# Performance work log

Measured on AMD Instinct MI355X. Metric: run time of the kernel, lower is better.

## Reference

```python
import jax, jax.numpy as jnp
import numpy as np

BLK = 128          # stk blocking
HID = 1024         # hidden_size
FFN = 4096         # ffn_hidden_size per expert
NE = 8             # moe_num_experts
TOK = 8192         # padded tokens (multiple of BLK)


def setup_inputs() -> dict:
    key = jax.random.key(0)
    k1, k2, k3 = jax.random.split(key, 3)
    x = jax.random.normal(k1, (TOK, HID), dtype=jnp.float32)
    w1 = jax.random.normal(k2, (NE * FFN, HID), dtype=jnp.float32) * 0.02
    n_row_blocks = TOK // BLK          # 64
    cols_per_expert = FFN // BLK       # 32
    # dMoE topology: each token row-block is assigned one expert; its nonzero
    # column blocks are all ffn blocks of that expert.
    expert_assign = jax.random.randint(k3, (n_row_blocks,), 0, NE)
    row_indices = jnp.repeat(jnp.arange(n_row_blocks), cols_per_expert)
    column_indices = (expert_assign[:, None] * cols_per_expert
                      + jnp.arange(cols_per_expert)[None, :]).reshape(-1)
    return {
        "x": x,
        "w1": w1,
        "row_indices": row_indices.astype(jnp.int32),     # [nnz]
        "column_indices": column_indices.astype(jnp.int32),  # [nnz]
        "block": BLK,
    }


def reference(x, w1, row_indices, column_indices, block):
    # sdd(x, w1.T, topo): out block k = x_block[row_indices[k]] @ w1_block[column_indices[k]].T
    hid = x.shape[1]
    xb = x.reshape(-1, block, hid)    # [n_row_blocks, blk, hid]
    wb = w1.reshape(-1, block, hid)   # [n_col_blocks, blk, hid]
    # [nnz, blk, blk] block-sparse data of the output matrix
    return jnp.einsum('kbh,kch->kbc', xb[row_indices], wb[column_indices])
```

## Files before the change

kernel.cpp:

```cpp
#include <hip/hip_runtime.h>
#include <hip/hip_bf16.h>
#include <stdint.h>

#define HID 1024
#define BLKDIM 128
#define BK 32
#define NK (HID / BK)

using short8 = __attribute__((ext_vector_type(8))) short;
using f32x4  = __attribute__((ext_vector_type(4))) float;

__device__ __forceinline__ uint32_t bfround(float f) {
    uint32_t u = __builtin_bit_cast(uint32_t, f);
    return (u + 0x7FFFu + ((u >> 16) & 1u)) >> 16;
}

__device__ __forceinline__ void gld16(const ushort* g, const ushort* lds_base) {
    __builtin_amdgcn_global_load_lds(
        (const __attribute__((address_space(1))) void*)g,
        (__attribute__((address_space(3))) void*)lds_base, 16, 0, 0);
}

__global__ __launch_bounds__(256)
void cvt_bf16_kernel(const float* __restrict__ src, uint4* __restrict__ dst, int n8) {
    int i = blockIdx.x * blockDim.x + threadIdx.x;
    if (i >= n8) return;
    const float4* s = reinterpret_cast<const float4*>(src) + (size_t)i * 2;
    float4 v0 = s[0], v1 = s[1];
    uint4 w;
    w.x = bfround(v0.x) | (bfround(v0.y) << 16);
    w.y = bfround(v0.z) | (bfround(v0.w) << 16);
    w.z = bfround(v1.x) | (bfround(v1.y) << 16);
    w.w = bfround(v1.z) | (bfround(v1.w) << 16);
    dst[i] = w;
}

__global__ __launch_bounds__(512, 2)
void sdd_pair_kernel(const ushort* __restrict__ xb, const ushort* __restrict__ wb,
                     const int* __restrict__ rind, const int* __restrict__ cind,
                     float* __restrict__ out) {
    __shared__ ushort sA[2][BLKDIM * BK];
    __shared__ ushort sB[2][2 * BLKDIM * BK];

    int g = blockIdx.x;
    const int nwg = gridDim.x;
    if ((nwg & 7) == 0) {
        const int cpx = nwg >> 3;
        g = (g & 7) * cpx + (g >> 3);
    }
    const int k0 = g * 2;
    const int r  = rind[k0];

    const int t = threadIdx.x;
    const int w = t >> 6;
    const int lane = t & 63;

    const int arow = w * 16 + (lane >> 2);
    const ushort* ag = xb + (size_t)(r * BLKDIM + arow) * HID + (lane & 3) * 8;
    const int brow0 = w * 32 + (lane >> 2);
    const int brow1 = brow0 + 16;
    const int cA = cind[k0 + (brow0 >> 7)];
    const int cB = cind[k0 + (brow1 >> 7)];
    const ushort* bg0 = wb + (size_t)(cA * BLKDIM + (brow0 & 127)) * HID + (lane & 3) * 8;
    const ushort* bg1 = wb + (size_t)(cB * BLKDIM + (brow1 & 127)) * HID + (lane & 3) * 8;

    const int wr = (w >> 2) * 64;
    const int wc = (w & 3) * 64;
    const int lr = lane & 15;
    const int lk = (lane >> 4) * 8;

    f32x4 acc[4][4];
#pragma unroll
    for (int m = 0; m < 4; ++m)
#pragma unroll
        for (int n = 0; n < 4; ++n)
            acc[m][n] = (f32x4){0.f, 0.f, 0.f, 0.f};

    auto stage = [&](int buf, int kt) {
        gld16(ag  + kt * BK, &sA[buf][w * 512]);
        gld16(bg0 + kt * BK, &sB[buf][w * 1024]);
        gld16(bg1 + kt * BK, &sB[buf][w * 1024 + 512]);
    };

    stage(0, 0);
    int cur = 0;
    for (int kt = 0; kt < NK; ++kt) {
        __syncthreads();
        if (kt + 1 < NK) stage(cur ^ 1, kt + 1);
        const ushort* sa = sA[cur];
        const ushort* sb = sB[cur];
        short8 aF[4], bF[4];
#pragma unroll
        for (int m = 0; m < 4; ++m)
            aF[m] = *reinterpret_cast<const short8*>(&sa[(wr + m * 16 + lr) * BK + lk]);
#pragma unroll
        for (int n = 0; n < 4; ++n)
            bF[n] = *reinterpret_cast<const short8*>(&sb[(wc + n * 16 + lr) * BK + lk]);
#pragma unroll
        for (int m = 0; m < 4; ++m)
#pragma unroll
            for (int n = 0; n < 4; ++n)
                acc[m][n] = __builtin_amdgcn_mfma_f32_16x16x32_bf16(aF[m], bF[n], acc[m][n], 0, 0, 0);
        cur ^= 1;
    }

    const int blk = (w & 3) >> 1;
    float* op = out + (size_t)(k0 + blk) * (BLKDIM * BLKDIM);
    const int colbase = (wc & 64) ? 64 : 0;
    const int rbase = wr + (lane >> 4) * 4;
#pragma unroll
    for (int m = 0; m < 4; ++m)
#pragma unroll
        for (int n = 0; n < 4; ++n) {
            const int col = colbase + n * 16 + lr;
#pragma unroll
            for (int j = 0; j < 4; ++j)
                op[(size_t)(rbase + m * 16 + j) * BLKDIM + col] = acc[m][n][j];
        }
}

__device__ __forceinline__ void store16f(ushort* dst, float4 v0, float4 v1, float4 v2, float4 v3) {
    uint4 w0, w1;
    w0.x = bfround(v0.x) | (bfround(v0.y) << 16);
    w0.y = bfround(v0.z) | (bfround(v0.w) << 16);
    w0.z = bfround(v1.x) | (bfround(v1.y) << 16);
    w0.w = bfround(v1.z) | (bfround(v1.w) << 16);
    w1.x = bfround(v2.x) | (bfround(v2.y) << 16);
    w1.y = bfround(v2.z) | (bfround(v2.w) << 16);
    w1.z = bfround(v3.x) | (bfround(v3.y) << 16);
    w1.w = bfround(v3.z) | (bfround(v3.w) << 16);
    uint4* d = reinterpret_cast<uint4*>(dst);
    d[0] = w0; d[1] = w1;
}

__global__ __launch_bounds__(256, 2)
void sdd_bf16_kernel(const float* __restrict__ x, const float* __restrict__ w1,
                     const int* __restrict__ rind, const int* __restrict__ cind,
                     float* __restrict__ out) {
    __shared__ ushort sA[2][BLKDIM * BK];
    __shared__ ushort sB[2][BLKDIM * BK];
    const int k = blockIdx.x;
    const int t = threadIdx.x;
    const int r = rind[k];
    const int c = cind[k];
    const float* Abase = x  + (size_t)r * BLKDIM * HID;
    const float* Bbase = w1 + (size_t)c * BLKDIM * HID;
    const int srow = t >> 1, shalf = t & 1;
    const float* aptr = Abase + (size_t)srow * HID + shalf * 16;
    const float* bptr = Bbase + (size_t)srow * HID + shalf * 16;
    const int soff = srow * BK + shalf * 16;
    const int wv = t >> 6, lane = t & 63;
    const int wr = (wv >> 1) * 64, wc = (wv & 1) * 64;
    const int lr = lane & 15, lk = (lane >> 4) * 8;
    f32x4 acc[4][4];
#pragma unroll
    for (int m = 0; m < 4; ++m)
#pragma unroll
        for (int n = 0; n < 4; ++n) acc[m][n] = (f32x4){0.f, 0.f, 0.f, 0.f};
    float4 ra[4], rb[4];
#pragma unroll
    for (int i = 0; i < 4; ++i) {
        ra[i] = *reinterpret_cast<const float4*>(aptr + i * 4);
        rb[i] = *reinterpret_cast<const float4*>(bptr + i * 4);
    }
    store16f(&sA[0][soff], ra[0], ra[1], ra[2], ra[3]);
    store16f(&sB[0][soff], rb[0], rb[1], rb[2], rb[3]);
    __syncthreads();
    for (int kt = 0; kt < NK; ++kt) {
        const int cur = kt & 1;
        if (kt + 1 < NK) {
            const float* ap = aptr + (kt + 1) * BK;
            const float* bp = bptr + (kt + 1) * BK;
#pragma unroll
            for (int i = 0; i < 4; ++i) {
                ra[i] = *reinterpret_cast<const float4*>(ap + i * 4);
                rb[i] = *reinterpret_cast<const float4*>(bp + i * 4);
            }
        }
        const ushort* sa = sA[cur];
        const ushort* sb = sB[cur];
        short8 aF[4], bF[4];
#pragma unroll
        for (int m = 0; m < 4; ++m) aF[m] = *reinterpret_cast<const short8*>(&sa[(wr + m * 16 + lr) * BK + lk]);
#pragma unroll
        for (int n = 0; n < 4; ++n) bF[n] = *reinterpret_cast<const short8*>(&sb[(wc + n * 16 + lr) * BK + lk]);
#pragma unroll
        for (int m = 0; m < 4; ++m)
#pragma unroll
            for (int n = 0; n < 4; ++n)
                acc[m][n] = __builtin_amdgcn_mfma_f32_16x16x32_bf16(aF[m], bF[n], acc[m][n], 0, 0, 0);
        if (kt + 1 < NK) {
            store16f(&sA[cur ^ 1][soff], ra[0], ra[1], ra[2], ra[3]);
            store16f(&sB[cur ^ 1][soff], rb[0], rb[1], rb[2], rb[3]);
        }
        __syncthreads();
    }
    float* op = out + (size_t)k * (BLKDIM * BLKDIM);
    const int rbase = wr + (lane >> 4) * 4;
#pragma unroll
    for (int m = 0; m < 4; ++m)
#pragma unroll
        for (int n = 0; n < 4; ++n) {
            const int col = wc + n * 16 + lr;
#pragma unroll
            for (int j = 0; j < 4; ++j)
                op[(size_t)(rbase + m * 16 + j) * BLKDIM + col] = acc[m][n][j];
        }
}

extern "C" void kernel_launch(void* const* d_in, const int* in_sizes, int n_in,
                              void* d_out, int out_size, void* d_ws, size_t ws_size,
                              hipStream_t stream) {
    const float* x  = (const float*)d_in[0];
    const float* w1 = (const float*)d_in[1];
    const int* ri   = (const int*)d_in[2];
    const int* ci   = (const int*)d_in[3];
    float* out      = (float*)d_out;
    const int nnz   = in_sizes[2];
    const int nx    = in_sizes[0];
    const int nw    = in_sizes[1];

    const size_t need = ((size_t)nx + (size_t)nw) * sizeof(ushort);
    if (ws_size >= need && (nnz & 1) == 0) {
        ushort* xb = (ushort*)d_ws;
        ushort* wb = xb + nx;
        const int nx8 = nx / 8, nw8 = nw / 8;
        hipLaunchKernelGGL(cvt_bf16_kernel, dim3((nx8 + 255) / 256), dim3(256), 0, stream,
                           x, (uint4*)xb, nx8);
        hipLaunchKernelGGL(cvt_bf16_kernel, dim3((nw8 + 255) / 256), dim3(256), 0, stream,
                           w1, (uint4*)wb, nw8);
        hipLaunchKernelGGL(sdd_pair_kernel, dim3(nnz / 2), dim3(512), 0, stream,
                           xb, wb, ri, ci, out);
    } else {
        hipLaunchKernelGGL(sdd_bf16_kernel, dim3(nnz), dim3(256), 0, stream,
                           x, w1, ri, ci, out);
    }
}
```

Baseline: 143.1 us.

## Triple-buffer LDS pipeline with BK=64, XOR swizzle and split MFMA phases

Reworks the pair GEMM kernel to a three-stage LDS ring with a K-tile of 64, prefetching two tiles ahead using direct global-to-LDS loads interleaved between two MFMA half-phases. An XOR swizzle on the loaded K chunk reduces LDS bank conflicts, and explicit vmcnt waits with raw s_barrier replace the per-iteration __syncthreads. s_setprio raises priority around the MFMA bursts. This roughly triples LDS use per workgroup (about 144KB), which may limit occupancy to one workgroup per CU despite launch bounds asking for two.

After: 155.0 us. +8.3%, slower.

```diff
diff --git a/kernel.cpp b/kernel.cpp
--- a/kernel.cpp
+++ b/kernel.cpp
@@ -4,8 +4,9 @@
 
 #define HID 1024
 #define BLKDIM 128
-#define BK 32
-#define NK (HID / BK)
+#define BKT 64
+#define NKT (HID / BKT)
+#define NBUF 3
 
 using short8 = __attribute__((ext_vector_type(8))) short;
 using f32x4  = __attribute__((ext_vector_type(4))) float;
@@ -36,11 +37,11 @@
 }
 
 __global__ __launch_bounds__(512, 2)
-void sdd_pair_kernel(const ushort* __restrict__ xb, const ushort* __restrict__ wb,
+void sdd_pipe_kernel(const ushort* __restrict__ xb, const ushort* __restrict__ wb,
                      const int* __restrict__ rind, const int* __restrict__ cind,
                      float* __restrict__ out) {
-    __shared__ ushort sA[2][BLKDIM * BK];
-    __shared__ ushort sB[2][2 * BLKDIM * BK];
+    __shared__ ushort sA[NBUF][BLKDIM * BKT];
+    __shared__ ushort sB[NBUF][2 * BLKDIM * BKT];
 
     int g = blockIdx.x;
     const int nwg = gridDim.x;
@@ -53,21 +54,25 @@
 
     const int t = threadIdx.x;
     const int w = t >> 6;
-    const int lane = t & 63;
-
-    const int arow = w * 16 + (lane >> 2);
-    const ushort* ag = xb + (size_t)(r * BLKDIM + arow) * HID + (lane & 3) * 8;
-    const int brow0 = w * 32 + (lane >> 2);
-    const int brow1 = brow0 + 16;
-    const int cA = cind[k0 + (brow0 >> 7)];
-    const int cB = cind[k0 + (brow1 >> 7)];
-    const ushort* bg0 = wb + (size_t)(cA * BLKDIM + (brow0 & 127)) * HID + (lane & 3) * 8;
-    const ushort* bg1 = wb + (size_t)(cB * BLKDIM + (brow1 & 127)) * HID + (lane & 3) * 8;
-
-    const int wr = (w >> 2) * 64;
-    const int wc = (w & 3) * 64;
-    const int lr = lane & 15;
-    const int lk = (lane >> 4) * 8;
+    const int l = t & 63;
+
+    const int kx = (((l & 7) ^ ((l >> 3) & 7)) * 8);
+    const ushort* agb = xb + (size_t)(r * BLKDIM + w * 16 + (l >> 3)) * HID + kx;
+    const int cblk = cind[k0 + (w >> 2)];
+    const ushort* bgb = wb + (size_t)(cblk * BLKDIM + ((w * 32) & 127) + (l >> 3)) * HID + kx;
+
+    const int wr   = (w >> 2) * 64;
+    const int wcol = (w & 3) * 64;
+    const int lr = l & 15;
+    const int s0 = (l >> 4) ^ (l & 7);
+    const int c0 = s0 * 8;
+    const int c1 = (s0 ^ 4) * 8;
+
+    int aoff[4], boff[4];
+#pragma unroll
+    for (int m = 0; m < 4; ++m) aoff[m] = (wr + m * 16 + lr) * BKT;
+#pragma unroll
+    for (int n = 0; n < 4; ++n) boff[n] = (wcol + n * 16 + lr) * BKT;
 
     f32x4 acc[4][4];
 #pragma unroll
@@ -76,38 +81,72 @@
         for (int n = 0; n < 4; ++n)
             acc[m][n] = (f32x4){0.f, 0.f, 0.f, 0.f};
 
-    auto stage = [&](int buf, int kt) {
-        gld16(ag  + kt * BK, &sA[buf][w * 512]);
-        gld16(bg0 + kt * BK, &sB[buf][w * 1024]);
-        gld16(bg1 + kt * BK, &sB[buf][w * 1024 + 512]);
+    auto stageA = [&](int b, int kt, int i) {
+        gld16(agb + (size_t)i * 8 * HID + kt * BKT, &sA[b][w * 1024 + i * 512]);
     };
-
-    stage(0, 0);
-    int cur = 0;
-    for (int kt = 0; kt < NK; ++kt) {
-        __syncthreads();
-        if (kt + 1 < NK) stage(cur ^ 1, kt + 1);
-        const ushort* sa = sA[cur];
-        const ushort* sb = sB[cur];
-        short8 aF[4], bF[4];
-#pragma unroll
-        for (int m = 0; m < 4; ++m)
-            aF[m] = *reinterpret_cast<const short8*>(&sa[(wr + m * 16 + lr) * BK + lk]);
-#pragma unroll
-        for (int n = 0; n < 4; ++n)
-            bF[n] = *reinterpret_cast<const short8*>(&sb[(wc + n * 16 + lr) * BK + lk]);
-#pragma unroll
-        for (int m = 0; m < 4; ++m)
+    auto stageB = [&](int b, int kt, int i) {
+        gld16(bgb + (size_t)i * 8 * HID + kt * BKT, &sB[b][w * 2048 + i * 512]);
+    };
+
+    stageA(0, 0, 0); stageA(0, 0, 1);
+    stageB(0, 0, 0); stageB(0, 0, 1); stageB(0, 0, 2); stageB(0, 0, 3);
+    stageA(1, 1, 0); stageA(1, 1, 1);
+    stageB(1, 1, 0); stageB(1, 1, 1); stageB(1, 1, 2); stageB(1, 1, 3);
+    asm volatile("s_waitcnt vmcnt(6)" ::: "memory");
+    __builtin_amdgcn_s_barrier();
+    __builtin_amdgcn_sched_barrier(0);
+
+    for (int kt = 0; kt < NKT; ++kt) {
+        const int cur = kt % 3;
+        const int nxt = (kt + 2) % 3;
+        const bool pre = (kt + 2) < NKT;
+        const ushort* sa = &sA[cur][0];
+        const ushort* sb = &sB[cur][0];
+
+        {
+            short8 aF[4], bF[4];
+#pragma unroll
+            for (int m = 0; m < 4; ++m)
+                aF[m] = *reinterpret_cast<const short8*>(&sa[aoff[m] + c0]);
 #pragma unroll
             for (int n = 0; n < 4; ++n)
-                acc[m][n] = __builtin_amdgcn_mfma_f32_16x16x32_bf16(aF[m], bF[n], acc[m][n], 0, 0, 0);
-        cur ^= 1;
+                bF[n] = *reinterpret_cast<const short8*>(&sb[boff[n] + c0]);
+            if (pre) { stageA(nxt, kt + 2, 0); stageB(nxt, kt + 2, 0); stageB(nxt, kt + 2, 1); }
+            __builtin_amdgcn_s_setprio(1);
+#pragma unroll
+            for (int m = 0; m < 4; ++m)
+#pragma unroll
+                for (int n = 0; n < 4; ++n)
+                    acc[m][n] = __builtin_amdgcn_mfma_f32_16x16x32_bf16(aF[m], bF[n], acc[m][n], 0, 0, 0);
+            __builtin_amdgcn_s_setprio(0);
+        }
+        {
+            short8 aF[4], bF[4];
+#pragma unroll
+            for (int m = 0; m < 4; ++m)
+                aF[m] = *reinterpret_cast<const short8*>(&sa[aoff[m] + c1]);
+#pragma unroll
+            for (int n = 0; n < 4; ++n)
+                bF[n] = *reinterpret_cast<const short8*>(&sb[boff[n] + c1]);
+            if (pre) { stageA(nxt, kt + 2, 1); stageB(nxt, kt + 2, 2); stageB(nxt, kt + 2, 3); }
+            __builtin_amdgcn_s_setprio(1);
+#pragma unroll
+            for (int m = 0; m < 4; ++m)
+#pragma unroll
+                for (int n = 0; n < 4; ++n)
+                    acc[m][n] = __builtin_amdgcn_mfma_f32_16x16x32_bf16(aF[m], bF[n], acc[m][n], 0, 0, 0);
+            __builtin_amdgcn_s_setprio(0);
+        }
+        if (pre) asm volatile("s_waitcnt vmcnt(6)" ::: "memory");
+        else     asm volatile("s_waitcnt vmcnt(0)" ::: "memory");
+        __builtin_amdgcn_s_barrier();
+        __builtin_amdgcn_sched_barrier(0);
     }
 
     const int blk = (w & 3) >> 1;
     float* op = out + (size_t)(k0 + blk) * (BLKDIM * BLKDIM);
-    const int colbase = (wc & 64) ? 64 : 0;
-    const int rbase = wr + (lane >> 4) * 4;
+    const int colbase = (wcol & 64) ? 64 : 0;
+    const int rbase = wr + (l >> 4) * 4;
 #pragma unroll
     for (int m = 0; m < 4; ++m)
 #pragma unroll
@@ -137,8 +176,8 @@
 void sdd_bf16_kernel(const float* __restrict__ x, const float* __restrict__ w1,
                      const int* __restrict__ rind, const int* __restrict__ cind,
                      float* __restrict__ out) {
-    __shared__ ushort sA[2][BLKDIM * BK];
-    __shared__ ushort sB[2][BLKDIM * BK];
+    __shared__ ushort sA[2][BLKDIM * 32];
+    __shared__ ushort sB[2][BLKDIM * 32];
     const int k = blockIdx.x;
     const int t = threadIdx.x;
     const int r = rind[k];
@@ -148,7 +187,7 @@
     const int srow = t >> 1, shalf = t & 1;
     const float* aptr = Abase + (size_t)srow * HID + shalf * 16;
     const float* bptr = Bbase + (size_t)srow * HID + shalf * 16;
-    const int soff = srow * BK + shalf * 16;
+    const int soff = srow * 32 + shalf * 16;
     const int wv = t >> 6, lane = t & 63;
     const int wr = (wv >> 1) * 64, wc = (wv & 1) * 64;
     const int lr = lane & 15, lk = (lane >> 4) * 8;
@@ -166,11 +205,11 @@
     store16f(&sA[0][soff], ra[0], ra[1], ra[2], ra[3]);
     store16f(&sB[0][soff], rb[0], rb[1], rb[2], rb[3]);
     __syncthreads();
-    for (int kt = 0; kt < NK; ++kt) {
+    for (int kt = 0; kt < 32; ++kt) {
         const int cur = kt & 1;
-        if (kt + 1 < NK) {
-            const float* ap = aptr + (kt + 1) * BK;
-            const float* bp = bptr + (kt + 1) * BK;
+        if (kt + 1 < 32) {
+            const float* ap = aptr + (kt + 1) * 32;
+            const float* bp = bptr + (kt + 1) * 32;
 #pragma unroll
             for (int i = 0; i < 4; ++i) {
                 ra[i] = *reinterpret_cast<const float4*>(ap + i * 4);
@@ -181,15 +220,15 @@
         const ushort* sb = sB[cur];
         short8 aF[4], bF[4];
 #pragma unroll
-        for (int m = 0; m < 4; ++m) aF[m] = *reinterpret_cast<const short8*>(&sa[(wr + m * 16 + lr) * BK + lk]);
-#pragma unroll
-        for (int n = 0; n < 4; ++n) bF[n] = *reinterpret_cast<const short8*>(&sb[(wc + n * 16 + lr) * BK + lk]);
+        for (int m = 0; m < 4; ++m) aF[m] = *reinterpret_cast<const short8*>(&sa[(wr + m * 16 + lr) * 32 + lk]);
+#pragma unroll
+        for (int n = 0; n < 4; ++n) bF[n] = *reinterpret_cast<const short8*>(&sb[(wc + n * 16 + lr) * 32 + lk]);
 #pragma unroll
         for (int m = 0; m < 4; ++m)
 #pragma unroll
             for (int n = 0; n < 4; ++n)
                 acc[m][n] = __builtin_amdgcn_mfma_f32_16x16x32_bf16(aF[m], bF[n], acc[m][n], 0, 0, 0);
-        if (kt + 1 < NK) {
+        if (kt + 1 < 32) {
             store16f(&sA[cur ^ 1][soff], ra[0], ra[1], ra[2], ra[3]);
             store16f(&sB[cur ^ 1][soff], rb[0], rb[1], rb[2], rb[3]);
         }
@@ -229,7 +268,7 @@
                            x, (uint4*)xb, nx8);
         hipLaunchKernelGGL(cvt_bf16_kernel, dim3((nw8 + 255) / 256), dim3(256), 0, stream,
                            w1, (uint4*)wb, nw8);
-        hipLaunchKernelGGL(sdd_pair_kernel, dim3(nnz / 2), dim3(512), 0, stream,
+        hipLaunchKernelGGL(sdd_pipe_kernel, dim3(nnz / 2), dim3(512), 0, stream,
                            xb, wb, ri, ci, out);
     } else {
         hipLaunchKernelGGL(sdd_bf16_kernel, dim3(nnz), dim3(256), 0, stream,
```
